# Kernel tuning notes

Hardware: AMD Instinct MI355X
Metric: run time of the kernel (lower is better)

Reference implementation:

```python
import jax, jax.numpy as jnp
import numpy as np

N = 100000
NNZ = 3200000
NFEAT, NHID, NCLASS = 512, 256, 41

def setup_inputs() -> dict:
    key = jax.random.key(0)
    ks = jax.random.split(key, 8)
    x = jax.random.normal(ks[0], (N, NFEAT), dtype=jnp.float32)
    adj_rows = jnp.sort(jax.random.randint(ks[1], (NNZ,), 0, N))
    adj_cols = jax.random.randint(ks[2], (NNZ,), 0, N)
    adj_vals = jax.random.uniform(ks[3], (NNZ,), dtype=jnp.float32) / 32.0  # ~normalized adj
    s1 = 1.0 / np.sqrt(NHID)
    s2 = 1.0 / np.sqrt(NCLASS)
    w1 = jax.random.uniform(ks[4], (NFEAT, NHID), minval=-s1, maxval=s1, dtype=jnp.float32)
    b1 = jax.random.uniform(ks[5], (NHID,), minval=-s1, maxval=s1, dtype=jnp.float32)
    w2 = jax.random.uniform(ks[6], (NHID, NCLASS), minval=-s2, maxval=s2, dtype=jnp.float32)
    b2 = jax.random.uniform(ks[7], (NCLASS,), minval=-s2, maxval=s2, dtype=jnp.float32)
    return {"x": x, "adj_rows": adj_rows, "adj_cols": adj_cols, "adj_vals": adj_vals,
            "w1": w1, "b1": b1, "w2": w2, "b2": b2}

def spmm(rows, cols, vals, dense):
    # sparse [N,N] @ dense [N,D] via gather + segment_sum
    gathered = dense[cols] * vals[:, None]  # [nnz, D]
    return jax.ops.segment_sum(gathered, rows, num_segments=N)

def reference(x, adj_rows, adj_cols, adj_vals, w1, b1, w2, b2):
    # layer 1: A(XW) + b, relu  (GraphConvolution)
    h = spmm(adj_rows, adj_cols, adj_vals, x @ w1) + b1
    h = jax.nn.relu(h)
    # dropout: inference mode (training=False) -> identity
    # layer 2: (AX)W + b  (GraphConvolution2)
    out = spmm(adj_rows, adj_cols, adj_vals, h) @ w2 + b2
    return jax.nn.log_softmax(out, axis=1)
```

## Files before the change

kernel.cpp:

```cpp
#include <hip/hip_runtime.h>
#include <math.h>

#define N_NODES 100000
#define NNZ_E   3200000
#define NFEAT   512
#define NHID    256
#define NCLASS  41
#define NC_PAD  48
#define P_STRIDE 64

typedef __attribute__((ext_vector_type(8))) short   short8;
typedef __attribute__((ext_vector_type(4))) float   f32x4;
typedef __attribute__((ext_vector_type(2))) float   f32x2;

typedef __attribute__((address_space(1))) const unsigned int gu32;
typedef __attribute__((address_space(3))) unsigned int lu32;

__device__ __forceinline__ unsigned short f2bf(float f) {
    unsigned u = __builtin_bit_cast(unsigned, f);
    unsigned r = u + 0x7fffu + ((u >> 16) & 1u);
    return (unsigned short)(r >> 16);
}
__device__ __forceinline__ unsigned char f2fp8(float f) {
    return (unsigned char)(__builtin_amdgcn_cvt_pk_fp8_f32(f, 0.f, 0, false) & 0xff);
}
__device__ __forceinline__ unsigned pk4(float a, float b, float c, float d) {
    unsigned u = __builtin_amdgcn_cvt_pk_fp8_f32(a, b, 0, false);
    return (unsigned)__builtin_amdgcn_cvt_pk_fp8_f32(c, d, (int)u, true);
}

__global__ __launch_bounds__(256) void prep_misc_kernel(const int* __restrict__ rows,
                                                        const float* __restrict__ w1,
                                                        const float* __restrict__ w2,
                                                        int* __restrict__ row_ptr,
                                                        unsigned char* __restrict__ w1q,
                                                        unsigned short* __restrict__ w2t) {
    int b = blockIdx.x;
    if (b < 392) {
        int r = b * 256 + threadIdx.x;
        if (r > N_NODES) return;
        int lo = 0, hi = NNZ_E;
        while (lo < hi) {
            int mid = (lo + hi) >> 1;
            if (rows[mid] < r) lo = mid + 1; else hi = mid;
        }
        row_ptr[r] = lo;
        return;
    }
    b -= 392;
    if (b < 512) {
        int tid = b * 256 + threadIdx.x;
        int n = tid >> 9, k = tid & 511;
        w1q[tid] = f2fp8(w1[k * NHID + n]);
        return;
    }
    b -= 512;
    {
        int t2 = b * 256 + threadIdx.x;
        int n = t2 >> 8, k = t2 & 255;
        w2t[t2] = (n < NCLASS) ? f2bf(w2[k * NCLASS + n]) : (unsigned short)0;
    }
}

__global__ __launch_bounds__(512) void gemm1_kernel(const float* __restrict__ x,
                                                    const unsigned char* __restrict__ w1q,
                                                    unsigned char* __restrict__ xw) {
    __shared__ unsigned char As[8192];
    __shared__ unsigned char Bs[16384];

    const int tid  = threadIdx.x;
    const int wv   = tid >> 6;
    const int lane = tid & 63;
    const int l15  = lane & 15;
    const int quad = lane >> 4;
    const int wvM  = wv >> 2;
    const int wvN  = wv & 3;
    const int rb   = blockIdx.x * 128;

    const int ar = tid >> 2;
    const int aq = tid & 3;
    int arow = rb + ar; if (arow >= N_NODES) arow = N_NODES - 1;
    const float* asrc = x + (long)arow * NFEAT + aq * 16;
    unsigned char* adst0 = As + ar * 64 + (((2 * aq + 0) ^ (ar & 6)) * 8);
    unsigned char* adst1 = As + ar * 64 + (((2 * aq + 1) ^ (ar & 6)) * 8);

    const int bn0 = (wv * 2 + 0) * 16 + (lane >> 2);
    const int bn1 = (wv * 2 + 1) * 16 + (lane >> 2);
    const int bg0 = (lane & 3) ^ ((bn0 >> 1) & 3);
    const int bg1 = (lane & 3) ^ ((bn1 >> 1) & 3);
    const unsigned char* bsrc0 = w1q + (long)bn0 * NFEAT + bg0 * 16;
    const unsigned char* bsrc1 = w1q + (long)bn1 * NFEAT + bg1 * 16;

    f32x4 acc[4][4] = {};

    float4 fr0 = *(const float4*)(asrc);
    float4 fr1 = *(const float4*)(asrc + 4);
    float4 fr2 = *(const float4*)(asrc + 8);
    float4 fr3 = *(const float4*)(asrc + 12);

    for (int c = 0; c < 8; c++) {
        const int kc = c * 64;
        __builtin_amdgcn_global_load_lds((gu32*)(bsrc0 + kc), (lu32*)(Bs + (wv * 2 + 0) * 1024), 16, 0, 0);
        __builtin_amdgcn_global_load_lds((gu32*)(bsrc1 + kc), (lu32*)(Bs + (wv * 2 + 1) * 1024), 16, 0, 0);
        unsigned u0 = pk4(fr0.x, fr0.y, fr0.z, fr0.w);
        unsigned u1 = pk4(fr1.x, fr1.y, fr1.z, fr1.w);
        unsigned u2 = pk4(fr2.x, fr2.y, fr2.z, fr2.w);
        unsigned u3 = pk4(fr3.x, fr3.y, fr3.z, fr3.w);
        *(unsigned long long*)adst0 = (unsigned long long)u0 | ((unsigned long long)u1 << 32);
        *(unsigned long long*)adst1 = (unsigned long long)u2 | ((unsigned long long)u3 << 32);
        if (c < 7) {
            fr0 = *(const float4*)(asrc + kc + 64);
            fr1 = *(const float4*)(asrc + kc + 68);
            fr2 = *(const float4*)(asrc + kc + 72);
            fr3 = *(const float4*)(asrc + kc + 76);
        }
        __syncthreads();

        unsigned long long a[4][2], b[4][2];
#pragma unroll
        for (int mt = 0; mt < 4; mt++) {
            int row = wvM * 64 + mt * 16 + l15;
#pragma unroll
            for (int ks = 0; ks < 2; ks++) {
                int p8 = (ks * 4 + quad) ^ (row & 6);
                a[mt][ks] = *(const unsigned long long*)(As + row * 64 + p8 * 8);
            }
        }
#pragma unroll
        for (int nt = 0; nt < 4; nt++) {
            int nr = wvN * 64 + nt * 16 + l15;
#pragma unroll
            for (int ks = 0; ks < 2; ks++) {
                int p8 = (ks * 4 + quad) ^ (nr & 6);
                b[nt][ks] = *(const unsigned long long*)(Bs + nr * 64 + p8 * 8);
            }
        }
#pragma unroll
        for (int ks = 0; ks < 2; ks++)
#pragma unroll
            for (int nt = 0; nt < 4; nt++)
#pragma unroll
                for (int mt = 0; mt < 4; mt++)
                    acc[mt][nt] = __builtin_amdgcn_mfma_f32_16x16x32_fp8_fp8(
                        (long)a[mt][ks], (long)b[nt][ks], acc[mt][nt], 0, 0, 0);
        __syncthreads();
    }

#pragma unroll
    for (int mt = 0; mt < 4; mt++) {
        int row0 = rb + wvM * 64 + mt * 16 + quad * 4;
#pragma unroll
        for (int nt = 0; nt < 4; nt++) {
            int col = wvN * 64 + nt * 16 + l15;
#pragma unroll
            for (int r = 0; r < 4; r++) {
                int row = row0 + r;
                if (row < N_NODES)
                    xw[(long)row * NHID + col] = f2fp8(acc[mt][nt][r]);
            }
        }
    }
}

__global__ __launch_bounds__(256) void spmm1g_kernel(const unsigned char* __restrict__ xw,
                                                     const int* __restrict__ row_ptr,
                                                     const int* __restrict__ cols,
                                                     const float* __restrict__ vals,
                                                     const float* __restrict__ b1,
                                                     const unsigned short* __restrict__ w2t,
                                                     unsigned char* __restrict__ p) {
    __shared__ unsigned short hl[32][264];

    const int wv   = threadIdx.x >> 6;
    const int lane = threadIdx.x & 63;
    const int row0 = blockIdx.x * 32;
    const float4 bv = *(const float4*)(b1 + lane * 4);

    for (int r = 0; r < 8; r++) {
        const int lrow = wv * 8 + r;
        const int row  = row0 + lrow;
        int e0 = row_ptr[row], e1 = row_ptr[row + 1];

        float a0 = 0.f, a1 = 0.f, a2 = 0.f, a3 = 0.f;
        for (int base = e0; base < e1; base += 64) {
            int   myc = 0;
            float myv = 0.f;
            int idx = base + lane;
            if (idx < e1) { myc = cols[idx]; myv = vals[idx]; }
            int cnt = e1 - base; if (cnt > 64) cnt = 64;
            int j = 0;
            for (; j + 8 <= cnt; j += 8) {
                int c[8]; float v[8];
#pragma unroll
                for (int u = 0; u < 8; u++) { c[u] = __shfl(myc, j + u); v[u] = __shfl(myv, j + u); }
                unsigned q[8];
#pragma unroll
                for (int u = 0; u < 8; u++) q[u] = *(const unsigned*)(xw + (long)c[u] * NHID + lane * 4);
#pragma unroll
                for (int u = 0; u < 8; u++) {
                    f32x2 lo = __builtin_amdgcn_cvt_pk_f32_fp8((int)q[u], false);
                    f32x2 hi = __builtin_amdgcn_cvt_pk_f32_fp8((int)q[u], true);
                    a0 += v[u] * lo[0];
                    a1 += v[u] * lo[1];
                    a2 += v[u] * hi[0];
                    a3 += v[u] * hi[1];
                }
            }
            for (; j < cnt; j++) {
                int   c = __shfl(myc, j);
                float v = __shfl(myv, j);
                unsigned q = *(const unsigned*)(xw + (long)c * NHID + lane * 4);
                f32x2 lo = __builtin_amdgcn_cvt_pk_f32_fp8((int)q, false);
                f32x2 hi = __builtin_amdgcn_cvt_pk_f32_fp8((int)q, true);
                a0 += v * lo[0];
                a1 += v * lo[1];
                a2 += v * hi[0];
                a3 += v * hi[1];
            }
        }
        a0 = fmaxf(a0 + bv.x, 0.f);
        a1 = fmaxf(a1 + bv.y, 0.f);
        a2 = fmaxf(a2 + bv.z, 0.f);
        a3 = fmaxf(a3 + bv.w, 0.f);
        unsigned lo32 = (unsigned)f2bf(a0) | ((unsigned)f2bf(a1) << 16);
        unsigned hi32 = (unsigned)f2bf(a2) | ((unsigned)f2bf(a3) << 16);
        unsigned* dst = (unsigned*)&hl[lrow][lane * 4];
        dst[0] = lo32;
        dst[1] = hi32;
    }
    __syncthreads();

    if (wv < 2) {
        const int l15 = lane & 15, quad = lane >> 4;
        f32x4 acc[3] = {};
#pragma unroll
        for (int kc = 0; kc < NHID; kc += 32) {
            short8 a = *(const short8*)(&hl[wv * 16 + l15][kc + quad * 8]);
#pragma unroll
            for (int nt = 0; nt < 3; nt++) {
                short8 b = *(const short8*)(w2t + (long)(nt * 16 + l15) * NHID + kc + quad * 8);
                acc[nt] = __builtin_amdgcn_mfma_f32_16x16x32_bf16(a, b, acc[nt], 0, 0, 0);
            }
        }
        const int prow0 = row0 + wv * 16 + quad * 4;
#pragma unroll
        for (int nt = 0; nt < 3; nt++) {
            int col = nt * 16 + l15;
#pragma unroll
            for (int r = 0; r < 4; r++)
                p[(long)(prow0 + r) * P_STRIDE + col] = f2fp8(acc[nt][r]);
        }
    }
}

__global__ __launch_bounds__(256) void spmm2_kernel(const unsigned char* __restrict__ p,
                                                    const int* __restrict__ row_ptr,
                                                    const int* __restrict__ cols,
                                                    const float* __restrict__ vals,
                                                    const float* __restrict__ b2,
                                                    float* __restrict__ out) {
    int row = blockIdx.x * 4 + (threadIdx.x >> 6);
    if (row >= N_NODES) return;
    int lane = threadIdx.x & 63;
    int e = lane >> 4;
    int t = lane & 15;
    int e0 = __builtin_amdgcn_readfirstlane(row_ptr[row]);
    int e1 = __builtin_amdgcn_readfirstlane(row_ptr[row + 1]);
    const unsigned toff = (unsigned)(t << 2);

    float a0 = 0.f, a1 = 0.f, a2 = 0.f, a3 = 0.f;
    if (e0 < e1) {
        const int em1 = e1 - 1;
        int i0 = e0 + e;     int i0c = i0 < e1 ? i0 : em1;
        int i1 = e0 + 4 + e; int i1c = i1 < e1 ? i1 : em1;
        int   ca = __builtin_nontemporal_load(cols + i0c);
        float va = __builtin_nontemporal_load(vals + i0c);
        int   cb = __builtin_nontemporal_load(cols + i1c);
        float vb = __builtin_nontemporal_load(vals + i1c);
        for (int j = e0; j < e1; j += 8) {
            int n0 = j + 8 + e;  int n0c = n0 < e1 ? n0 : em1;
            int n1 = j + 12 + e; int n1c = n1 < e1 ? n1 : em1;
            int   cc = __builtin_nontemporal_load(cols + n0c);
            float vc = __builtin_nontemporal_load(vals + n0c);
            int   cd = __builtin_nontemporal_load(cols + n1c);
            float vd = __builtin_nontemporal_load(vals + n1c);
            unsigned q0 = (t < 12) ? *(const unsigned*)(p + (long)ca * P_STRIDE + toff) : 0u;
            unsigned q1 = (t < 12) ? *(const unsigned*)(p + (long)cb * P_STRIDE + toff) : 0u;
            float v0 = (j + e     < e1) ? va : 0.f;
            float v1 = (j + 4 + e < e1) ? vb : 0.f;
            f32x2 lo0 = __builtin_amdgcn_cvt_pk_f32_fp8((int)q0, false);
            f32x2 hi0 = __builtin_amdgcn_cvt_pk_f32_fp8((int)q0, true);
            f32x2 lo1 = __builtin_amdgcn_cvt_pk_f32_fp8((int)q1, false);
            f32x2 hi1 = __builtin_amdgcn_cvt_pk_f32_fp8((int)q1, true);
            a0 += v0 * lo0[0]; a1 += v0 * lo0[1]; a2 += v0 * hi0[0]; a3 += v0 * hi0[1];
            a0 += v1 * lo1[0]; a1 += v1 * lo1[1]; a2 += v1 * hi1[0]; a3 += v1 * hi1[1];
            ca = cc; va = vc; cb = cd; vb = vd;
        }
    }
    a0 += __shfl_xor(a0, 16); a1 += __shfl_xor(a1, 16);
    a2 += __shfl_xor(a2, 16); a3 += __shfl_xor(a3, 16);
    a0 += __shfl_xor(a0, 32); a1 += __shfl_xor(a1, 32);
    a2 += __shfl_xor(a2, 32); a3 += __shfl_xor(a3, 32);

    int c0 = 4 * t, c1 = 4 * t + 1, c2 = 4 * t + 2, c3 = 4 * t + 3;
    float l0 = (c0 < NCLASS) ? a0 + b2[c0] : -__builtin_inff();
    float l1 = (c1 < NCLASS) ? a1 + b2[c1] : -__builtin_inff();
    float l2 = (c2 < NCLASS) ? a2 + b2[c2] : -__builtin_inff();
    float l3 = (c3 < NCLASS) ? a3 + b2[c3] : -__builtin_inff();
    float m = fmaxf(fmaxf(l0, l1), fmaxf(l2, l3));
#pragma unroll
    for (int s = 8; s; s >>= 1) m = fmaxf(m, __shfl_xor(m, s));
    float esum = ((c0 < NCLASS) ? __expf(l0 - m) : 0.f)
               + ((c1 < NCLASS) ? __expf(l1 - m) : 0.f)
               + ((c2 < NCLASS) ? __expf(l2 - m) : 0.f)
               + ((c3 < NCLASS) ? __expf(l3 - m) : 0.f);
#pragma unroll
    for (int s = 8; s; s >>= 1) esum += __shfl_xor(esum, s);
    float lse = m + __logf(esum);
    if (e == 0) {
        long ob = (long)row * NCLASS;
        if (c0 < NCLASS) out[ob + c0] = l0 - lse;
        if (c1 < NCLASS) out[ob + c1] = l1 - lse;
        if (c2 < NCLASS) out[ob + c2] = l2 - lse;
        if (c3 < NCLASS) out[ob + c3] = l3 - lse;
    }
}

extern "C" void kernel_launch(void* const* d_in, const int* in_sizes, int n_in,
                              void* d_out, int out_size, void* d_ws, size_t ws_size,
                              hipStream_t stream) {
    const float* x        = (const float*)d_in[0];
    const int*   adj_rows = (const int*)  d_in[1];
    const int*   adj_cols = (const int*)  d_in[2];
    const float* adj_vals = (const float*)d_in[3];
    const float* w1       = (const float*)d_in[4];
    const float* b1       = (const float*)d_in[5];
    const float* w2       = (const float*)d_in[6];
    const float* b2       = (const float*)d_in[7];
    float* out = (float*)d_out;

    char* ws = (char*)d_ws;
    unsigned char*  w1q     = (unsigned char*) (ws);
    unsigned short* w2t     = (unsigned short*)(ws + 0x20000);
    int*            row_ptr = (int*)           (ws + 0x26000);
    unsigned char*  p       = (unsigned char*) (ws + 0x90000);
    unsigned char*  xw      = (unsigned char*) (ws + 0x3180000);

    prep_misc_kernel<<<392 + 512 + 48, 256, 0, stream>>>(adj_rows, w1, w2, row_ptr, w1q, w2t);
    gemm1_kernel<<<(N_NODES + 127) / 128, 512, 0, stream>>>(x, w1q, xw);
    spmm1g_kernel<<<N_NODES / 32, 256, 0, stream>>>(xw, row_ptr, adj_cols, adj_vals, b1, w2t, p);
    spmm2_kernel<<<(N_NODES + 3) / 4, 256, 0, stream>>>(p, row_ptr, adj_cols, adj_vals, b2, out);
}
```

Measured before the change: 555.8 us.

## Split wavefront into half-waves gathering two edges with 8-byte loads and prefetch

```diff
diff --git a/kernel.cpp b/kernel.cpp
--- a/kernel.cpp
+++ b/kernel.cpp
@@ -12,6 +12,7 @@
 typedef __attribute__((ext_vector_type(8))) short   short8;
 typedef __attribute__((ext_vector_type(4))) float   f32x4;
 typedef __attribute__((ext_vector_type(2))) float   f32x2;
+typedef __attribute__((ext_vector_type(2))) unsigned int u32x2;
 
 typedef __attribute__((address_space(1))) const unsigned int gu32;
 typedef __attribute__((address_space(3))) unsigned int lu32;
@@ -173,60 +174,96 @@
 
     const int wv   = threadIdx.x >> 6;
     const int lane = threadIdx.x & 63;
+    const int e    = lane >> 5;
+    const int t    = lane & 31;
     const int row0 = blockIdx.x * 32;
-    const float4 bv = *(const float4*)(b1 + lane * 4);
+    const unsigned toff = (unsigned)(t << 3);
+
+    const float4 bv0 = *(const float4*)(b1 + t * 8);
+    const float4 bv1 = *(const float4*)(b1 + t * 8 + 4);
 
     for (int r = 0; r < 8; r++) {
         const int lrow = wv * 8 + r;
         const int row  = row0 + lrow;
-        int e0 = row_ptr[row], e1 = row_ptr[row + 1];
+        int e0 = __builtin_amdgcn_readfirstlane(row_ptr[row]);
+        int e1 = __builtin_amdgcn_readfirstlane(row_ptr[row + 1]);
 
         float a0 = 0.f, a1 = 0.f, a2 = 0.f, a3 = 0.f;
-        for (int base = e0; base < e1; base += 64) {
-            int   myc = 0;
-            float myv = 0.f;
-            int idx = base + lane;
-            if (idx < e1) { myc = cols[idx]; myv = vals[idx]; }
-            int cnt = e1 - base; if (cnt > 64) cnt = 64;
-            int j = 0;
-            for (; j + 8 <= cnt; j += 8) {
-                int c[8]; float v[8];
-#pragma unroll
-                for (int u = 0; u < 8; u++) { c[u] = __shfl(myc, j + u); v[u] = __shfl(myv, j + u); }
-                unsigned q[8];
-#pragma unroll
-                for (int u = 0; u < 8; u++) q[u] = *(const unsigned*)(xw + (long)c[u] * NHID + lane * 4);
-#pragma unroll
-                for (int u = 0; u < 8; u++) {
-                    f32x2 lo = __builtin_amdgcn_cvt_pk_f32_fp8((int)q[u], false);
-                    f32x2 hi = __builtin_amdgcn_cvt_pk_f32_fp8((int)q[u], true);
-                    a0 += v[u] * lo[0];
-                    a1 += v[u] * lo[1];
-                    a2 += v[u] * hi[0];
-                    a3 += v[u] * hi[1];
-                }
-            }
-            for (; j < cnt; j++) {
-                int   c = __shfl(myc, j);
-                float v = __shfl(myv, j);
-                unsigned q = *(const unsigned*)(xw + (long)c * NHID + lane * 4);
-                f32x2 lo = __builtin_amdgcn_cvt_pk_f32_fp8((int)q, false);
-                f32x2 hi = __builtin_amdgcn_cvt_pk_f32_fp8((int)q, true);
-                a0 += v * lo[0];
-                a1 += v * lo[1];
-                a2 += v * hi[0];
-                a3 += v * hi[1];
-            }
-        }
-        a0 = fmaxf(a0 + bv.x, 0.f);
-        a1 = fmaxf(a1 + bv.y, 0.f);
-        a2 = fmaxf(a2 + bv.z, 0.f);
-        a3 = fmaxf(a3 + bv.w, 0.f);
-        unsigned lo32 = (unsigned)f2bf(a0) | ((unsigned)f2bf(a1) << 16);
-        unsigned hi32 = (unsigned)f2bf(a2) | ((unsigned)f2bf(a3) << 16);
-        unsigned* dst = (unsigned*)&hl[lrow][lane * 4];
-        dst[0] = lo32;
-        dst[1] = hi32;
+        float a4 = 0.f, a5 = 0.f, a6 = 0.f, a7 = 0.f;
+        if (e0 < e1) {
+            const int em1 = e1 - 1;
+            int i0 = e0 + e;     int i0c = i0 < e1 ? i0 : em1;
+            int i1 = e0 + 2 + e; int i1c = i1 < e1 ? i1 : em1;
+            int i2 = e0 + 4 + e; int i2c = i2 < e1 ? i2 : em1;
+            int i3 = e0 + 6 + e; int i3c = i3 < e1 ? i3 : em1;
+            int   ca = __builtin_nontemporal_load(cols + i0c);
+            float va = __builtin_nontemporal_load(vals + i0c);
+            int   cb = __builtin_nontemporal_load(cols + i1c);
+            float vb = __builtin_nontemporal_load(vals + i1c);
+            int   cc = __builtin_nontemporal_load(cols + i2c);
+            float vc = __builtin_nontemporal_load(vals + i2c);
+            int   cd = __builtin_nontemporal_load(cols + i3c);
+            float vd = __builtin_nontemporal_load(vals + i3c);
+            for (int j = e0; j < e1; j += 8) {
+                int n0 = j + 8 + e;  int n0c = n0 < e1 ? n0 : em1;
+                int n1 = j + 10 + e; int n1c = n1 < e1 ? n1 : em1;
+                int n2 = j + 12 + e; int n2c = n2 < e1 ? n2 : em1;
+                int n3 = j + 14 + e; int n3c = n3 < e1 ? n3 : em1;
+                int   ce = __builtin_nontemporal_load(cols + n0c);
+                float ve = __builtin_nontemporal_load(vals + n0c);
+                int   cf = __builtin_nontemporal_load(cols + n1c);
+                float vf = __builtin_nontemporal_load(vals + n1c);
+                int   cg = __builtin_nontemporal_load(cols + n2c);
+                float vg = __builtin_nontemporal_load(vals + n2c);
+                int   ch = __builtin_nontemporal_load(cols + n3c);
+                float vh = __builtin_nontemporal_load(vals + n3c);
+                u32x2 q0 = *(const u32x2*)(xw + (long)ca * NHID + toff);
+                u32x2 q1 = *(const u32x2*)(xw + (long)cb * NHID + toff);
+                u32x2 q2 = *(const u32x2*)(xw + (long)cc * NHID + toff);
+                u32x2 q3 = *(const u32x2*)(xw + (long)cd * NHID + toff);
+                float v0 = (j + e     < e1) ? va : 0.f;
+                float v1 = (j + 2 + e < e1) ? vb : 0.f;
+                float v2 = (j + 4 + e < e1) ? vc : 0.f;
+                float v3 = (j + 6 + e < e1) ? vd : 0.f;
+#define ACC8(q, v) do { \
+                f32x2 lo0_ = __builtin_amdgcn_cvt_pk_f32_fp8((int)(q).x, false); \
+                f32x2 hi0_ = __builtin_amdgcn_cvt_pk_f32_fp8((int)(q).x, true);  \
+                f32x2 lo1_ = __builtin_amdgcn_cvt_pk_f32_fp8((int)(q).y, false); \
+                f32x2 hi1_ = __builtin_amdgcn_cvt_pk_f32_fp8((int)(q).y, true);  \
+                a0 += (v) * lo0_[0]; a1 += (v) * lo0_[1]; \
+                a2 += (v) * hi0_[0]; a3 += (v) * hi0_[1]; \
+                a4 += (v) * lo1_[0]; a5 += (v) * lo1_[1]; \
+                a6 += (v) * hi1_[0]; a7 += (v) * hi1_[1]; } while (0)
+                ACC8(q0, v0);
+                ACC8(q1, v1);
+                ACC8(q2, v2);
+                ACC8(q3, v3);
+#undef ACC8
+                ca = ce; va = ve; cb = cf; vb = vf;
+                cc = cg; vc = vg; cd = ch; vd = vh;
+            }
+        }
+        a0 += __shfl_xor(a0, 32); a1 += __shfl_xor(a1, 32);
+        a2 += __shfl_xor(a2, 32); a3 += __shfl_xor(a3, 32);
+        a4 += __shfl_xor(a4, 32); a5 += __shfl_xor(a5, 32);
+        a6 += __shfl_xor(a6, 32); a7 += __shfl_xor(a7, 32);
+
+        if (e == 0) {
+            a0 = fmaxf(a0 + bv0.x, 0.f);
+            a1 = fmaxf(a1 + bv0.y, 0.f);
+            a2 = fmaxf(a2 + bv0.z, 0.f);
+            a3 = fmaxf(a3 + bv0.w, 0.f);
+            a4 = fmaxf(a4 + bv1.x, 0.f);
+            a5 = fmaxf(a5 + bv1.y, 0.f);
+            a6 = fmaxf(a6 + bv1.z, 0.f);
+            a7 = fmaxf(a7 + bv1.w, 0.f);
+            uint4 o;
+            o.x = (unsigned)f2bf(a0) | ((unsigned)f2bf(a1) << 16);
+            o.y = (unsigned)f2bf(a2) | ((unsigned)f2bf(a3) << 16);
+            o.z = (unsigned)f2bf(a4) | ((unsigned)f2bf(a5) << 16);
+            o.w = (unsigned)f2bf(a6) | ((unsigned)f2bf(a7) << 16);
+            *(uint4*)(&hl[lrow][t * 8]) = o;
+        }
     }
     __syncthreads();
 
```

New measurement: 583.5 us. 1.05x slower.
